# Optimization experiments

Hardware: AMD Instinct MI355X
Metric: run time of the kernel (lower is better)

Reference implementation:

```python
import jax, jax.numpy as jnp
import numpy as np

EPS = 1e-8

def _cos_loss(a, b):
    # faithful to torch cos_loss: norm = sqrt(sum(x*x)), x / (norm + 1e-8)
    a_norm = jnp.sqrt(jnp.sum(a * a, axis=1, keepdims=True))
    b_norm = jnp.sqrt(jnp.sum(b * b, axis=1, keepdims=True))
    a_n = a / (a_norm + EPS)
    b_n = b / (b_norm + EPS)
    cossim = jnp.sum(a_n * b_n, axis=1)
    return jnp.mean(1.0 - cossim)

def setup_inputs() -> dict:
    key = jax.random.key(0)
    k1, k2, k3 = jax.random.split(key, 3)
    shape = (1, 768, 64, 64)  # [n, c_cat(block2 VGG16 feats), h, w]
    a = jax.random.normal(k1, shape, dtype=jnp.float32)
    b = jax.random.normal(k2, shape, dtype=jnp.float32)
    d = jax.random.normal(k3, shape, dtype=jnp.float32)
    return {"a": a, "b": b, "d": d}

def reference(a, b, d):
    n, c, h, w = a.shape
    hw = h * w
    a_flat = a.reshape(n, c, hw)   # [n, c, hw]
    b_flat = b.reshape(n, c, hw)   # [n, c, h2w2]
    d_flat = d.reshape(n, c, hw)
    # normalize exactly as argmin_cos_distance: sqrt(sum + 1e-8) then /(norm + 1e-8)
    b_norm = jnp.sqrt(jnp.sum(b_flat * b_flat, axis=1, keepdims=True) + EPS)
    b_n = b_flat / (b_norm + EPS)
    a_norm = jnp.sqrt(jnp.sum(a_flat * a_flat, axis=1, keepdims=True) + EPS)
    a_n = a_flat / (a_norm + EPS)
    # cosine distance matrix [n, hw, h2w2]
    d_mat = 1.0 - jnp.einsum('ncp,ncq->npq', a_n, b_n)
    z_best = jnp.argmin(d_mat, axis=2)  # [n, hw]
    # gather matched style features from d
    idx = jnp.broadcast_to(z_best[:, None, :], (n, c, hw))
    target_feats = jnp.take_along_axis(d_flat, idx, axis=2)  # [n, c, hw]
    # NNFM loss between rendered feats and matched style feats (score is detached)
    loss = _cos_loss(a_flat, target_feats)
    z_new = target_feats.reshape(n, c, h, w)
    return (loss, z_new, z_best)
```

## Files before the change

### kernel.cpp

```cpp
#include <hip/hip_runtime.h>
#include <math.h>

#define EPS  1e-8f
#define C    768
#define HW   4096
#define NKB  24
#define NNB  12
#define NBN  32
#define TAU  0.016f
#define NCH_NEW 12
#define NCH_OLD 48

typedef float  floatx4 __attribute__((ext_vector_type(4)));
typedef short  shortx8 __attribute__((ext_vector_type(8)));
typedef unsigned short ushort_t;
typedef unsigned int   uint_t;
typedef __attribute__((address_space(1))) uint_t as1_uint;
typedef __attribute__((address_space(3))) uint_t as3_uint;

__device__ __forceinline__ ushort_t f2bf(float v) {
    uint_t u = __float_as_uint(v);
    uint_t r = (u + 0x7FFFu + ((u >> 16) & 1u)) >> 16;
    return (ushort_t)r;
}
__device__ __forceinline__ void async_cp16(const ushort_t* g, ushort_t* l) {
    __builtin_amdgcn_global_load_lds((const as1_uint*)g, (as3_uint*)l, 16, 0, 0);
}

__global__ __launch_bounds__(256) void prep_kernel(
    const float* __restrict__ a, const float* __restrict__ b,
    const float* __restrict__ d,
    ushort_t* __restrict__ Ah, ushort_t* __restrict__ Bh,
    float* __restrict__ dT, float* __restrict__ bT,
    float* __restrict__ nbp2, float* __restrict__ out)
{
    __shared__ float tile[64][65];
    const int t = threadIdx.x;
    const int p0 = blockIdx.x * 64;
    const int c0 = blockIdx.y * 64;
    const int x = t & 63, y4 = t >> 6;
    const int pl = t >> 2, g = t & 3;
    const int pg = p0 + pl;
    const int sw = (pg >> 1) & 3;

    if (blockIdx.x == 0 && blockIdx.y == 0 && t == 0) out[0] = 0.f;

#pragma unroll
    for (int i = 0; i < 16; ++i) {
        int c = y4 * 16 + i;
        tile[c][x] = d[(size_t)(c0 + c) * HW + p0 + x];
    }
    __syncthreads();
#pragma unroll
    for (int i = 0; i < 16; ++i) {
        int p = y4 * 16 + i;
        dT[(size_t)(p0 + p) * C + c0 + x] = tile[x][p];
    }
    __syncthreads();

#pragma unroll
    for (int i = 0; i < 16; ++i) {
        int c = y4 * 16 + i;
        tile[c][x] = b[(size_t)(c0 + c) * HW + p0 + x];
    }
    __syncthreads();
#pragma unroll
    for (int i = 0; i < 16; ++i) {
        int p = y4 * 16 + i;
        bT[(size_t)(p0 + p) * C + c0 + x] = tile[x][p];
    }
#pragma unroll
    for (int h = 0; h < 2; ++h) {
        const int kb = (c0 >> 5) + h;
        uint_t w[4];
#pragma unroll
        for (int u = 0; u < 4; ++u) {
            ushort_t lo = f2bf(tile[h * 32 + g * 8 + 2 * u][pl]);
            ushort_t hi = f2bf(tile[h * 32 + g * 8 + 2 * u + 1][pl]);
            w[u] = (uint_t)lo | ((uint_t)hi << 16);
        }
        uint4* oh = (uint4*)(Bh + ((size_t)kb * HW + pg) * 32);
        oh[g ^ sw] = make_uint4(w[0], w[1], w[2], w[3]);
    }
    if (t < 64) {
        float s = 0.f;
#pragma unroll
        for (int c = 0; c < 64; ++c) { float v = tile[c][t]; s += v * v; }
        nbp2[blockIdx.y * HW + p0 + t] = s;
    }
    __syncthreads();

#pragma unroll
    for (int i = 0; i < 16; ++i) {
        int c = y4 * 16 + i;
        tile[c][x] = a[(size_t)(c0 + c) * HW + p0 + x];
    }
    __syncthreads();
#pragma unroll
    for (int h = 0; h < 2; ++h) {
        const int kb = (c0 >> 5) + h;
        uint_t w[4];
#pragma unroll
        for (int u = 0; u < 4; ++u) {
            ushort_t lo = f2bf(tile[h * 32 + g * 8 + 2 * u][pl]);
            ushort_t hi = f2bf(tile[h * 32 + g * 8 + 2 * u + 1][pl]);
            w[u] = (uint_t)lo | ((uint_t)hi << 16);
        }
        uint4* oh = (uint4*)(Ah + ((size_t)kb * HW + pg) * 32);
        oh[g ^ sw] = make_uint4(w[0], w[1], w[2], w[3]);
    }
}

__global__ __launch_bounds__(256, 4) void gemm_mfma_kernel(
    const ushort_t* __restrict__ Ah, const ushort_t* __restrict__ Bh,
    const float* __restrict__ nbp2,
    float* __restrict__ pv1, int* __restrict__ pi1,
    float* __restrict__ pv2, int* __restrict__ pi2)
{
    __shared__ __align__(16) char smem[16896];
    ushort_t* sA  = (ushort_t*)smem;
    ushort_t* sB  = (ushort_t*)(smem + 8192);
    float*    nb_s = (float*)(smem + 16384);

    const int tid  = threadIdx.x;
    const int lane = tid & 63;
    const int wave = tid >> 6;
    const int wm = wave >> 1, wn = wave & 1;
    const int bm = blockIdx.x, bn = blockIdx.y;
    const int l15 = lane & 15, l4 = lane >> 4;
    const int swz = (l15 >> 1) & 3;

    if (tid < 128) {
        float s = 0.f;
        int q = bn * 128 + tid;
#pragma unroll
        for (int ch = 0; ch < NNB; ++ch) s += nbp2[ch * HW + q];
        nb_s[tid] = 1.0f / (sqrtf(s + EPS) + EPS);
    }

    floatx4 acc[4][4];
#pragma unroll
    for (int i = 0; i < 4; ++i)
#pragma unroll
        for (int j = 0; j < 4; ++j) acc[i][j] = (floatx4){0.f, 0.f, 0.f, 0.f};

    for (int kb = 0; kb < NKB; ++kb) {
        const size_t aoff = (size_t)(kb * HW + bm * 128) * 32 + tid * 8;
        const size_t boff = (size_t)(kb * HW + bn * 128) * 32 + tid * 8;
        async_cp16(Ah + aoff,        sA + tid * 8);
        async_cp16(Ah + aoff + 2048, sA + tid * 8 + 2048);
        async_cp16(Bh + boff,        sB + tid * 8);
        async_cp16(Bh + boff + 2048, sB + tid * 8 + 2048);
        __syncthreads();

        shortx8 af[4], bf_[4];
#pragma unroll
        for (int i = 0; i < 4; ++i)
            af[i] = *(const shortx8*)&sA[((wm * 4 + i) * 16 + l15) * 32 + ((l4 ^ swz) * 8)];
#pragma unroll
        for (int j = 0; j < 4; ++j)
            bf_[j] = *(const shortx8*)&sB[((wn * 4 + j) * 16 + l15) * 32 + ((l4 ^ swz) * 8)];
#pragma unroll
        for (int i = 0; i < 4; ++i)
#pragma unroll
            for (int j = 0; j < 4; ++j)
                acc[i][j] = __builtin_amdgcn_mfma_f32_16x16x32_bf16(af[i], bf_[j], acc[i][j], 0, 0, 0);
        __syncthreads();
    }

    float rnb[4];
#pragma unroll
    for (int j = 0; j < 4; ++j)
        rnb[j] = nb_s[wn * 64 + j * 16 + l15];

    float* lv1 = (float*)smem;
    int*   li1 = (int*)(smem + 1024);
    float* lv2 = (float*)(smem + 2048);
    int*   li2 = (int*)(smem + 3072);

#pragma unroll
    for (int i = 0; i < 4; ++i) {
#pragma unroll
        for (int r = 0; r < 4; ++r) {
            float v1 = -INFINITY, v2 = -INFINITY; int i1 = 0, i2 = 0;
#pragma unroll
            for (int j = 0; j < 4; ++j) {
                float sv = acc[i][j][r] * rnb[j];
                int q = bn * 128 + wn * 64 + j * 16 + l15;
                if (sv > v1) { v2 = v1; i2 = i1; v1 = sv; i1 = q; }
                else if (sv > v2) { v2 = sv; i2 = q; }
            }
#pragma unroll
            for (int m = 1; m < 16; m <<= 1) {
                float ov1 = __shfl_xor(v1, m, 64);
                int   oi1 = __shfl_xor(i1, m, 64);
                float ov2 = __shfl_xor(v2, m, 64);
                int   oi2 = __shfl_xor(i2, m, 64);
                if (ov1 > v1 || (ov1 == v1 && oi1 < i1)) {
                    if (v1 > ov2 || (v1 == ov2 && i1 < oi2)) { v2 = v1; i2 = i1; }
                    else { v2 = ov2; i2 = oi2; }
                    v1 = ov1; i1 = oi1;
                } else if (ov1 > v2 || (ov1 == v2 && oi1 < i2)) {
                    v2 = ov1; i2 = oi1;
                }
            }
            if (l15 == 0) {
                int pl = wm * 64 + i * 16 + l4 * 4 + r;
                lv1[pl * 2 + wn] = v1; li1[pl * 2 + wn] = i1;
                lv2[pl * 2 + wn] = v2; li2[pl * 2 + wn] = i2;
            }
        }
    }
    __syncthreads();
    if (tid < 128) {
        float v1 = lv1[tid * 2],     v2 = lv2[tid * 2];
        int   i1 = li1[tid * 2],     i2 = li2[tid * 2];
        float w1 = lv1[tid * 2 + 1], w2 = lv2[tid * 2 + 1];
        int   j1 = li1[tid * 2 + 1], j2 = li2[tid * 2 + 1];
        if (w1 > v1 || (w1 == v1 && j1 < i1)) {
            if (v1 > w2 || (v1 == w2 && i1 < j2)) { v2 = v1; i2 = i1; }
            else { v2 = w2; i2 = j2; }
            v1 = w1; i1 = j1;
        } else if (w1 > v2 || (w1 == v2 && j1 < i2)) {
            v2 = w1; i2 = j1;
        }
        int p = bm * 128 + tid;
        pv1[p * NBN + bn] = v1; pi1[p * NBN + bn] = i1;
        pv2[p * NBN + bn] = v2; pi2[p * NBN + bn] = i2;
    }
}

__global__ __launch_bounds__(256) void reduce_recheck_kernel(
    const float* __restrict__ a, const float* __restrict__ b,
    const float* __restrict__ bT, int bt_ok,
    const float* __restrict__ pv1, const int* __restrict__ pi1,
    const float* __restrict__ pv2, const int* __restrict__ pi2,
    int* __restrict__ zb, float* __restrict__ out_zbest)
{
    const int wave = threadIdx.x >> 6, lane = threadIdx.x & 63;
    const int p = blockIdx.x * 4 + wave;
    const int tq = lane & 31;

    float v1, v2; int i1, cand;
    if (lane < 32) {
        v1 = pv1[p * NBN + tq]; i1 = pi1[p * NBN + tq]; v2 = pv2[p * NBN + tq];
        cand = i1;
    } else {
        v1 = -INFINITY; v2 = -INFINITY; i1 = 0x7fffffff;
        cand = pi2[p * NBN + tq];
    }
#pragma unroll
    for (int m = 1; m < 32; m <<= 1) {
        float ov1 = __shfl_xor(v1, m, 64);
        int   oi1 = __shfl_xor(i1, m, 64);
        float ov2 = __shfl_xor(v2, m, 64);
        if (ov1 > v1 || (ov1 == v1 && oi1 < i1)) {
            v2 = fmaxf(v1, ov2); v1 = ov1; i1 = oi1;
        } else {
            v2 = fmaxf(v2, ov1);
        }
    }
    v1 = __shfl(v1, 0, 64); v2 = __shfl(v2, 0, 64); i1 = __shfl(i1, 0, 64);

    if (v1 - v2 >= TAU) {
        if (lane == 0) { zb[p] = i1; out_zbest[p] = (float)i1; }
        return;
    }

    int q = cand;
    float dot = 0.f, b2 = 0.f;
    if (bt_ok) {
        const float* br = bT + (size_t)q * C;
        const float* ap = a + p;
#pragma unroll 4
        for (int c = 0; c < C; c += 4) {
            float4 bv = *(const float4*)(br + c);
            dot += ap[(size_t)c * HW] * bv.x + ap[(size_t)(c + 1) * HW] * bv.y
                 + ap[(size_t)(c + 2) * HW] * bv.z + ap[(size_t)(c + 3) * HW] * bv.w;
            b2  += bv.x * bv.x + bv.y * bv.y + bv.z * bv.z + bv.w * bv.w;
        }
    } else {
#pragma unroll 8
        for (int c = 0; c < C; ++c) {
            float av = a[c * HW + p];
            float bv = b[c * HW + q];
            dot += av * bv; b2 += bv * bv;
        }
    }
    float s = dot / (sqrtf(b2 + EPS) + EPS);
#pragma unroll
    for (int m = 1; m < 64; m <<= 1) {
        float os = __shfl_xor(s, m, 64);
        int   oq = __shfl_xor(q, m, 64);
        if (os > s || (os == s && oq < q)) { s = os; q = oq; }
    }
    if (lane == 0) { zb[p] = q; out_zbest[p] = (float)q; }
}

__global__ __launch_bounds__(256) void gather_loss_kernel(
    const float* __restrict__ a, const float* __restrict__ dT,
    const int* __restrict__ zb, float* __restrict__ out,
    float* __restrict__ pdot, float* __restrict__ pa2, float* __restrict__ pt2)
{
    __shared__ float tile[64][65];
    __shared__ int qs[64];
    const int t = threadIdx.x;
    const int p0 = blockIdx.x * 64;
    const int c0 = blockIdx.y * 64;
    if (t < 64) qs[t] = zb[p0 + t];
    __syncthreads();

    {
        const int pl = t >> 2, sub = t & 3;
        const float* src = dT + (size_t)qs[pl] * C + c0 + sub * 16;
        float4 v0 = *(const float4*)(src);
        float4 v1 = *(const float4*)(src + 4);
        float4 v2 = *(const float4*)(src + 8);
        float4 v3 = *(const float4*)(src + 12);
        float* dst = &tile[pl][sub * 16];
        dst[0] = v0.x; dst[1] = v0.y; dst[2]  = v0.z; dst[3]  = v0.w;
        dst[4] = v1.x; dst[5] = v1.y; dst[6]  = v1.z; dst[7]  = v1.w;
        dst[8] = v2.x; dst[9] = v2.y; dst[10] = v2.z; dst[11] = v2.w;
        dst[12] = v3.x; dst[13] = v3.y; dst[14] = v3.z; dst[15] = v3.w;
    }
    __syncthreads();

    const int p = t & 63, cg = t >> 6;
    float dot = 0.f, a2 = 0.f, t2 = 0.f;
#pragma unroll
    for (int i = 0; i < 16; ++i) {
        int cc = cg * 16 + i;
        float tv = tile[p][cc];
        float av = a[(size_t)(c0 + cc) * HW + p0 + p];
        out[1 + (size_t)(c0 + cc) * HW + p0 + p] = tv;
        dot += av * tv; a2 += av * av; t2 += tv * tv;
    }
    __shared__ float r1[256], r2[256], r3[256];
    r1[t] = dot; r2[t] = a2; r3[t] = t2;
    __syncthreads();
    if (t < 64) {
        dot = r1[t] + r1[t + 64] + r1[t + 128] + r1[t + 192];
        a2  = r2[t] + r2[t + 64] + r2[t + 128] + r2[t + 192];
        t2  = r3[t] + r3[t + 64] + r3[t + 128] + r3[t + 192];
        pdot[blockIdx.y * HW + p0 + t] = dot;
        pa2[blockIdx.y * HW + p0 + t]  = a2;
        pt2[blockIdx.y * HW + p0 + t]  = t2;
    }
}

__global__ __launch_bounds__(256) void loss_finalize_kernel(
    const float* __restrict__ pdot, const float* __restrict__ pa2,
    const float* __restrict__ pt2, float* __restrict__ out, int nch)
{
    int p = blockIdx.x * 256 + threadIdx.x;
    float dot = 0.f, a2 = 0.f, t2 = 0.f;
#pragma unroll 12
    for (int ch = 0; ch < nch; ++ch) {
        dot += pdot[ch * HW + p];
        a2  += pa2[ch * HW + p];
        t2  += pt2[ch * HW + p];
    }
    float cs = dot / ((sqrtf(a2) + EPS) * (sqrtf(t2) + EPS));
    float contrib = 1.f - cs;
    __shared__ float red[256];
    red[threadIdx.x] = contrib;
    __syncthreads();
    for (int s = 128; s > 0; s >>= 1) {
        if (threadIdx.x < s) red[threadIdx.x] += red[threadIdx.x + s];
        __syncthreads();
    }
    if (threadIdx.x == 0) atomicAdd(out, red[0] * (1.0f / HW));
}

__global__ __launch_bounds__(256) void bnorm_partial_fb_kernel(
    const float* __restrict__ b, float* __restrict__ nbp)
{
    int q = blockIdx.x * 256 + threadIdx.x;
    int c0 = blockIdx.y * 32;
    float s = 0.f;
#pragma unroll 8
    for (int c = c0; c < c0 + 32; ++c) { float v = b[c * HW + q]; s += v * v; }
    nbp[blockIdx.y * HW + q] = s;
}

__global__ __launch_bounds__(256) void bnorm_finalize_fb_kernel(
    const float* __restrict__ nbp, float* __restrict__ nb)
{
    int q = blockIdx.x * 256 + threadIdx.x;
    float s = 0.f;
#pragma unroll
    for (int ch = 0; ch < NKB; ++ch) s += nbp[ch * HW + q];
    nb[q] = sqrtf(s + EPS) + EPS;
}

__global__ __launch_bounds__(256) void gemm_argmax_fb_kernel(
    const float* __restrict__ A, const float* __restrict__ B,
    const float* __restrict__ nb,
    float* __restrict__ pval, int* __restrict__ pidx)
{
    __shared__ __align__(16) char smem[16384];
    float (*As)[128] = (float (*)[128])smem;
    float (*Bs)[128] = (float (*)[128])(smem + 4096);
    const int m0 = blockIdx.x * 128, q0 = blockIdx.y * 128;
    const int tid = threadIdx.x;
    const int tx = tid & 15, ty = tid >> 4;
    const int lr = tid >> 5, lc = (tid & 31) * 4;
    float acc[8][8] = {};
    for (int k0 = 0; k0 < C; k0 += 8) {
        *(float4*)&As[lr][lc] = *(const float4*)&A[(k0 + lr) * HW + m0 + lc];
        *(float4*)&Bs[lr][lc] = *(const float4*)&B[(k0 + lr) * HW + q0 + lc];
        __syncthreads();
#pragma unroll
        for (int kk = 0; kk < 8; ++kk) {
            float a8[8], b8[8];
            *(float4*)&a8[0] = *(float4*)&As[kk][ty * 8];
            *(float4*)&a8[4] = *(float4*)&As[kk][ty * 8 + 4];
            *(float4*)&b8[0] = *(float4*)&Bs[kk][tx * 8];
            *(float4*)&b8[4] = *(float4*)&Bs[kk][tx * 8 + 4];
#pragma unroll
            for (int i = 0; i < 8; ++i)
#pragma unroll
                for (int j = 0; j < 8; ++j) acc[i][j] += a8[i] * b8[j];
        }
        __syncthreads();
    }
    float nbv[8];
#pragma unroll
    for (int j = 0; j < 8; ++j) nbv[j] = nb[q0 + tx * 8 + j];
    float (*rv)[16] = (float (*)[16])smem;
    int   (*ri)[16] = (int   (*)[16])(smem + 8192);
#pragma unroll
    for (int i = 0; i < 8; ++i) {
        float bv = -INFINITY; int bi = 0;
#pragma unroll
        for (int j = 0; j < 8; ++j) {
            float s = acc[i][j] / nbv[j];
            int q = q0 + tx * 8 + j;
            if (s > bv) { bv = s; bi = q; }
        }
        rv[ty * 8 + i][tx] = bv;
        ri[ty * 8 + i][tx] = bi;
    }
    __syncthreads();
    if (tid < 128) {
        float bv = rv[tid][0]; int bi = ri[tid][0];
#pragma unroll
        for (int t = 1; t < 16; ++t) {
            float v = rv[tid][t]; int ii = ri[tid][t];
            if (v > bv || (v == bv && ii < bi)) { bv = v; bi = ii; }
        }
        pval[(m0 + tid) * NBN + blockIdx.y] = bv;
        pidx[(m0 + tid) * NBN + blockIdx.y] = bi;
    }
}

__global__ __launch_bounds__(256) void reduce_fb_kernel(
    const float* __restrict__ pval, const int* __restrict__ pidx,
    int* __restrict__ zb, float* __restrict__ out_zbest)
{
    int p = blockIdx.x * 256 + threadIdx.x;
    float bv = pval[p * NBN]; int bi = pidx[p * NBN];
#pragma unroll 8
    for (int t = 1; t < NBN; ++t) {
        float v = pval[p * NBN + t]; int ii = pidx[p * NBN + t];
        if (v > bv || (v == bv && ii < bi)) { bv = v; bi = ii; }
    }
    zb[p] = bi;
    out_zbest[p] = (float)bi;
}

__global__ __launch_bounds__(256) void gather_partial_kernel(
    const float* __restrict__ a, const float* __restrict__ d,
    const int* __restrict__ zb, float* __restrict__ out,
    float* __restrict__ pdot, float* __restrict__ pa2, float* __restrict__ pt2)
{
    int p = blockIdx.x * 256 + threadIdx.x;
    int ch = blockIdx.y;
    int c0 = ch * (C / NCH_OLD);
    int q = zb[p];
    float dot = 0.f, a2 = 0.f, t2 = 0.f;
#pragma unroll
    for (int c = c0; c < c0 + C / NCH_OLD; ++c) {
        float av = a[c * HW + p];
        float tv = d[c * HW + q];
        dot += av * tv; a2 += av * av; t2 += tv * tv;
        out[1 + c * HW + p] = tv;
    }
    pdot[ch * HW + p] = dot;
    pa2[ch * HW + p] = a2;
    pt2[ch * HW + p] = t2;
}

extern "C" void kernel_launch(void* const* d_in, const int* in_sizes, int n_in,
                              void* d_out, int out_size, void* d_ws, size_t ws_size,
                              hipStream_t stream) {
    const float* a = (const float*)d_in[0];
    const float* b = (const float*)d_in[1];
    const float* d = (const float*)d_in[2];
    float* out = (float*)d_out;
    float* out_zbest = out + 1 + (size_t)C * HW;

    char* ws = (char*)d_ws;
    size_t off = 0;
    auto alloc = [&](size_t bytes) { void* p = ws + off; off = (off + bytes + 255) & ~(size_t)255; return p; };

    const size_t PACK = (size_t)C * HW * 2;
    ushort_t* Ah = (ushort_t*)alloc(PACK);
    ushort_t* Bh = (ushort_t*)alloc(PACK);
    float* nbp = (float*)alloc((size_t)NKB * HW * 4);
    float* pv1 = (float*)alloc((size_t)HW * NBN * 4);
    int*   pi1 = (int*)alloc((size_t)HW * NBN * 4);
    float* pv2 = (float*)alloc((size_t)HW * NBN * 4);
    int*   pi2 = (int*)alloc((size_t)HW * NBN * 4);
    int*   zb  = (int*)alloc(HW * 4);
    float* pdot = (float*)alloc((size_t)NCH_NEW * HW * 4);
    float* pa2  = (float*)alloc((size_t)NCH_NEW * HW * 4);
    float* pt2  = (float*)alloc((size_t)NCH_NEW * HW * 4);
    float* dT  = (float*)alloc((size_t)C * HW * 4);
    float* bT  = (float*)alloc((size_t)C * HW * 4);
    bool fast = off <= ws_size;

    if (fast) {
        prep_kernel<<<dim3(HW / 64, C / 64), 256, 0, stream>>>(
            a, b, d, Ah, Bh, dT, bT, nbp, out);
        gemm_mfma_kernel<<<dim3(HW / 128, HW / 128), 256, 0, stream>>>(
            Ah, Bh, nbp, pv1, pi1, pv2, pi2);
        reduce_recheck_kernel<<<HW / 4, 256, 0, stream>>>(
            a, b, bT, 1, pv1, pi1, pv2, pi2, zb, out_zbest);
        gather_loss_kernel<<<dim3(HW / 64, NCH_NEW), 256, 0, stream>>>(
            a, dT, zb, out, pdot, pa2, pt2);
        loss_finalize_kernel<<<HW / 256, 256, 0, stream>>>(pdot, pa2, pt2, out, NCH_NEW);
    } else {
        off = 0;
        float* nb = (float*)alloc(HW * 4);
        nbp = (float*)alloc((size_t)NKB * HW * 4);
        pv1 = (float*)alloc((size_t)HW * NBN * 4);
        pi1 = (int*)alloc((size_t)HW * NBN * 4);
        zb  = (int*)alloc(HW * 4);
        float* pdot2 = (float*)alloc((size_t)NCH_OLD * HW * 4);
        float* pa22  = (float*)alloc((size_t)NCH_OLD * HW * 4);
        float* pt22  = (float*)alloc((size_t)NCH_OLD * HW * 4);
        hipMemsetAsync(d_out, 0, sizeof(float), stream);
        bnorm_partial_fb_kernel<<<dim3(HW / 256, NKB), 256, 0, stream>>>(b, nbp);
        bnorm_finalize_fb_kernel<<<HW / 256, 256, 0, stream>>>(nbp, nb);
        gemm_argmax_fb_kernel<<<dim3(HW / 128, HW / 128), 256, 0, stream>>>(a, b, nb, pv1, pi1);
        reduce_fb_kernel<<<HW / 256, 256, 0, stream>>>(pv1, pi1, zb, out_zbest);
        gather_partial_kernel<<<dim3(HW / 256, NCH_OLD), 256, 0, stream>>>(
            a, d, zb, out, pdot2, pa22, pt22);
        loss_finalize_kernel<<<HW / 256, 256, 0, stream>>>(pdot2, pa22, pt22, out, NCH_OLD);
    }
}
```

Baseline: 182.6 us.

## Double-buffer GEMM shared-memory tiles to overlap async loads with MFMA

Splits the shared-memory staging area into two A/B buffers and prefetches the next K-block with async copies while MFMAs run on the current one. The nb-norm reduction is also moved after the first prefetch so its global loads overlap with it. This aims to hide global-to-LDS latency that the single-buffer loop exposed on every K step. In exchange, LDS use roughly doubles per block, which may lower occupancy under the 4-blocks-per-SM launch bound.

```diff
diff --git a/kernel.cpp b/kernel.cpp
--- a/kernel.cpp
+++ b/kernel.cpp
@@ -117,10 +117,12 @@
     float* __restrict__ pv1, int* __restrict__ pi1,
     float* __restrict__ pv2, int* __restrict__ pi2)
 {
-    __shared__ __align__(16) char smem[16896];
-    ushort_t* sA  = (ushort_t*)smem;
-    ushort_t* sB  = (ushort_t*)(smem + 8192);
-    float*    nb_s = (float*)(smem + 16384);
+    __shared__ __align__(16) char smem[33280];
+    ushort_t* sA0 = (ushort_t*)smem;
+    ushort_t* sB0 = (ushort_t*)(smem + 8192);
+    ushort_t* sA1 = (ushort_t*)(smem + 16384);
+    ushort_t* sB1 = (ushort_t*)(smem + 24576);
+    float*    nb_s = (float*)(smem + 32768);
 
     const int tid  = threadIdx.x;
     const int lane = tid & 63;
@@ -130,6 +132,36 @@
     const int l15 = lane & 15, l4 = lane >> 4;
     const int swz = (l15 >> 1) & 3;
 
+    floatx4 acc[4][4];
+#pragma unroll
+    for (int i = 0; i < 4; ++i)
+#pragma unroll
+        for (int j = 0; j < 4; ++j) acc[i][j] = (floatx4){0.f, 0.f, 0.f, 0.f};
+
+    auto stage = [&](int kb, ushort_t* dA, ushort_t* dB) {
+        const size_t aoff = (size_t)(kb * HW + bm * 128) * 32 + tid * 8;
+        const size_t boff = (size_t)(kb * HW + bn * 128) * 32 + tid * 8;
+        async_cp16(Ah + aoff,        dA + tid * 8);
+        async_cp16(Ah + aoff + 2048, dA + tid * 8 + 2048);
+        async_cp16(Bh + boff,        dB + tid * 8);
+        async_cp16(Bh + boff + 2048, dB + tid * 8 + 2048);
+    };
+    auto compute = [&](const ushort_t* pA, const ushort_t* pB) {
+        shortx8 af[4], bf_[4];
+#pragma unroll
+        for (int i = 0; i < 4; ++i)
+            af[i] = *(const shortx8*)&pA[((wm * 4 + i) * 16 + l15) * 32 + ((l4 ^ swz) * 8)];
+#pragma unroll
+        for (int j = 0; j < 4; ++j)
+            bf_[j] = *(const shortx8*)&pB[((wn * 4 + j) * 16 + l15) * 32 + ((l4 ^ swz) * 8)];
+#pragma unroll
+        for (int i = 0; i < 4; ++i)
+#pragma unroll
+            for (int j = 0; j < 4; ++j)
+                acc[i][j] = __builtin_amdgcn_mfma_f32_16x16x32_bf16(af[i], bf_[j], acc[i][j], 0, 0, 0);
+    };
+
+    stage(0, sA0, sB0);
     if (tid < 128) {
         float s = 0.f;
         int q = bn * 128 + tid;
@@ -137,34 +169,14 @@
         for (int ch = 0; ch < NNB; ++ch) s += nbp2[ch * HW + q];
         nb_s[tid] = 1.0f / (sqrtf(s + EPS) + EPS);
     }
-
-    floatx4 acc[4][4];
-#pragma unroll
-    for (int i = 0; i < 4; ++i)
-#pragma unroll
-        for (int j = 0; j < 4; ++j) acc[i][j] = (floatx4){0.f, 0.f, 0.f, 0.f};
-
-    for (int kb = 0; kb < NKB; ++kb) {
-        const size_t aoff = (size_t)(kb * HW + bm * 128) * 32 + tid * 8;
-        const size_t boff = (size_t)(kb * HW + bn * 128) * 32 + tid * 8;
-        async_cp16(Ah + aoff,        sA + tid * 8);
-        async_cp16(Ah + aoff + 2048, sA + tid * 8 + 2048);
-        async_cp16(Bh + boff,        sB + tid * 8);
-        async_cp16(Bh + boff + 2048, sB + tid * 8 + 2048);
+    __syncthreads();
+
+    for (int kb = 0; kb < NKB; kb += 2) {
+        stage(kb + 1, sA1, sB1);
+        compute(sA0, sB0);
         __syncthreads();
-
-        shortx8 af[4], bf_[4];
-#pragma unroll
-        for (int i = 0; i < 4; ++i)
-            af[i] = *(const shortx8*)&sA[((wm * 4 + i) * 16 + l15) * 32 + ((l4 ^ swz) * 8)];
-#pragma unroll
-        for (int j = 0; j < 4; ++j)
-            bf_[j] = *(const shortx8*)&sB[((wn * 4 + j) * 16 + l15) * 32 + ((l4 ^ swz) * 8)];
-#pragma unroll
-        for (int i = 0; i < 4; ++i)
-#pragma unroll
-            for (int j = 0; j < 4; ++j)
-                acc[i][j] = __builtin_amdgcn_mfma_f32_16x16x32_bf16(af[i], bf_[j], acc[i][j], 0, 0, 0);
+        if (kb + 2 < NKB) stage(kb + 2, sA0, sB0);
+        compute(sA1, sB1);
         __syncthreads();
     }
 
```

After: 180.2 us. About the same (-1.3%).
